# Kernel optimization log

Hardware: AMD Instinct MI355X
Metric: run time of the kernel (lower is better)

Reference implementation:

```python
import jax, jax.numpy as jnp
import numpy as np

KERNEL_SIZE = 10
CHANNELS = 3
MEAN = (KERNEL_SIZE - 1) // 2  # 4


def setup_inputs() -> dict:
    key = jax.random.key(0)
    x = jax.random.uniform(key, (32, CHANNELS, 512, 512), dtype=jnp.float32)
    return {"x": x}


def reference(x) -> jnp.ndarray:
    # (1 - x) * 0.5, then replicate pad by MEAN on H and W
    y = (1.0 - x) * 0.5
    y = jnp.pad(y, ((0, 0), (0, 0), (MEAN, MEAN), (MEAN, MEAN)), mode="edge")
    # depthwise (groups=channels) conv with all-ones 10x10 kernel, VALID padding
    # weight layout OIHW with O=CHANNELS, I=1 (feature_group_count=CHANNELS)
    w = jnp.ones((CHANNELS, 1, KERNEL_SIZE, KERNEL_SIZE), dtype=x.dtype)
    out = jax.lax.conv_general_dilated(
        y, w,
        window_strides=(1, 1),
        padding="VALID",
        dimension_numbers=("NCHW", "OIHW", "NCHW"),
        feature_group_count=CHANNELS,
    )
    return out  # [B, C, H-1, W-1]
```

## Files before the change

kernel.cpp:

```cpp
#include <hip/hip_runtime.h>


#define IMG 512
#define OUTW 511
#define KS 10
#define MEAN 4
#define BAND 64
#define TSTREAM (BAND + KS - 1)

__global__ __launch_bounds__(256, 8) void onedilate_kernel(
    const float* __restrict__ x, float* __restrict__ out)
{
    const int t = threadIdx.x;
    const int c = blockIdx.x * 256 + t;
    const int rb = blockIdx.y * BAND;
    const int bc = blockIdx.z;

    const float* __restrict__ xim = x + (size_t)bc * IMG * IMG;
    float* __restrict__ oim = out + (size_t)bc * OUTW * OUTW;

    int cc[KS];
    #pragma unroll
    for (int k = 0; k < KS; ++k)
        cc[k] = min(max(c - MEAN + k, 0), IMG - 1);

    float h[KS];
    #pragma unroll
    for (int k = 0; k < KS; ++k) h[k] = 0.0f;
    float V = 0.0f;

    const bool cok = (c < OUTW);

    for (int t0 = 0; t0 < TSTREAM; t0 += KS) {
        #pragma unroll
        for (int u = 0; u < KS; ++u) {
            int s = t0 + u;
            if (s < TSTREAM) {
                int ri = min(max(rb + s - MEAN, 0), IMG - 1);
                const float* __restrict__ rowp = xim + ri * IMG;
                float H = 0.0f;
                #pragma unroll
                for (int k = 0; k < KS; ++k) H += rowp[cc[k]];
                V += H - h[u];
                h[u] = H;
                int i = rb + s - (KS - 1);
                if (s >= KS - 1 && i < OUTW && cok)
                    oim[i * OUTW + c] = 50.0f - 0.5f * V;
            }
        }
    }
}

extern "C" void kernel_launch(void* const* d_in, const int* in_sizes, int n_in,
                              void* d_out, int out_size, void* d_ws, size_t ws_size,
                              hipStream_t stream) {
    const float* x = (const float*)d_in[0];
    float* out = (float*)d_out;

    dim3 block(256, 1, 1);
    dim3 grid(2,
              IMG / BAND,
              32 * 3);
    onedilate_kernel<<<grid, block, 0, stream>>>(x, out);
}
```

Baseline: 215.6 us.

## Compute four output columns per thread with float4 row loads and sliding sums

Each thread now handles four adjacent output columns, loading three float4 vectors plus one scalar per input row and deriving the four horizontal window sums incrementally instead of doing ten scalar gathers per column. Row bands shrink to 32 rows per half-block, with two sub-bands per 256-thread block covering 64 rows. The aim is fewer load instructions and less redundant horizontal summation. The cost is more vertical halo recomputation per band, and output stores are now strided scalar writes of four floats per thread, since the 511-wide output rows are not 16-byte aligned.

```diff
diff --git a/kernel.cpp b/kernel.cpp
--- a/kernel.cpp
+++ b/kernel.cpp
@@ -5,31 +5,35 @@
 #define OUTW 511
 #define KS 10
 #define MEAN 4
-#define BAND 64
-#define TSTREAM (BAND + KS - 1)
+#define SUB 32
+#define TSTREAM (SUB + KS - 1)
 
-__global__ __launch_bounds__(256, 8) void onedilate_kernel(
+__global__ __launch_bounds__(256) void onedilate_kernel(
     const float* __restrict__ x, float* __restrict__ out)
 {
-    const int t = threadIdx.x;
-    const int c = blockIdx.x * 256 + t;
-    const int rb = blockIdx.y * BAND;
-    const int bc = blockIdx.z;
+    const int tid = threadIdx.x;
+    const int j   = tid & 127;
+    const int sub = tid >> 7;
+    const int rb  = blockIdx.x * 64 + sub * SUB;
+    const int bc  = blockIdx.y;
 
     const float* __restrict__ xim = x + (size_t)bc * IMG * IMG;
     float* __restrict__ oim = out + (size_t)bc * OUTW * OUTW;
 
-    int cc[KS];
+    const int b0  = 4 * j - 4;
+    const int bl0 = max(b0, 0);
+    const int b2  = 4 * j + 4;
+    const int bl2 = min(b2, IMG - 4);
+    const bool lo0 = (b0 < 0);
+    const bool hi2 = (b2 > IMG - 4);
+    const int c12 = min(4 * j + 8, IMG - 1);
+
+    float4 ring[KS];
     #pragma unroll
-    for (int k = 0; k < KS; ++k)
-        cc[k] = min(max(c - MEAN + k, 0), IMG - 1);
+    for (int k = 0; k < KS; ++k) ring[k] = make_float4(0.f, 0.f, 0.f, 0.f);
+    float4 V = make_float4(0.f, 0.f, 0.f, 0.f);
 
-    float h[KS];
-    #pragma unroll
-    for (int k = 0; k < KS; ++k) h[k] = 0.0f;
-    float V = 0.0f;
-
-    const bool cok = (c < OUTW);
+    const int cbase = 4 * j;
 
     for (int t0 = 0; t0 < TSTREAM; t0 += KS) {
         #pragma unroll
@@ -38,14 +42,39 @@
             if (s < TSTREAM) {
                 int ri = min(max(rb + s - MEAN, 0), IMG - 1);
                 const float* __restrict__ rowp = xim + ri * IMG;
-                float H = 0.0f;
-                #pragma unroll
-                for (int k = 0; k < KS; ++k) H += rowp[cc[k]];
-                V += H - h[u];
-                h[u] = H;
-                int i = rb + s - (KS - 1);
-                if (s >= KS - 1 && i < OUTW && cok)
-                    oim[i * OUTW + c] = 50.0f - 0.5f * V;
+
+                float4 v0 = *(const float4*)(rowp + bl0);
+                float4 v1 = *(const float4*)(rowp + cbase);
+                float4 v2 = *(const float4*)(rowp + bl2);
+                float w12 = rowp[c12];
+                if (lo0) v0 = make_float4(v0.x, v0.x, v0.x, v0.x);
+                if (hi2) v2 = make_float4(v2.w, v2.w, v2.w, v2.w);
+
+                float S = v0.x + v0.y + v0.z + v0.w
+                        + v1.x + v1.y + v1.z + v1.w
+                        + v2.x + v2.y;
+                float4 H;
+                H.x = S;
+                S += v2.z - v0.x; H.y = S;
+                S += v2.w - v0.y; H.z = S;
+                S += w12  - v0.z; H.w = S;
+
+                V.x += H.x - ring[u].x;
+                V.y += H.y - ring[u].y;
+                V.z += H.z - ring[u].z;
+                V.w += H.w - ring[u].w;
+                ring[u] = H;
+
+                if (s >= KS - 1) {
+                    int i = rb + s - (KS - 1);
+                    if (i < OUTW) {
+                        float* op = oim + (size_t)i * OUTW + cbase;
+                        op[0] = 50.0f - 0.5f * V.x;
+                        op[1] = 50.0f - 0.5f * V.y;
+                        op[2] = 50.0f - 0.5f * V.z;
+                        if (cbase + 3 < OUTW) op[3] = 50.0f - 0.5f * V.w;
+                    }
+                }
             }
         }
     }
@@ -58,8 +87,8 @@
     float* out = (float*)d_out;
 
     dim3 block(256, 1, 1);
-    dim3 grid(2,
-              IMG / BAND,
-              32 * 3);
+    dim3 grid(IMG / 64,
+              32 * 3,
+              1);
     onedilate_kernel<<<grid, block, 0, stream>>>(x, out);
 }
```

Result: faster. 190.5 us (-11.7%).
